# Kernel optimization log

Measured on AMD Instinct MI355X. Metric: run time of the kernel, lower is better.

## Reference

```python
import jax, jax.numpy as jnp
import numpy as np


def setup_inputs() -> dict:
    key = jax.random.key(0)
    k1, k2, k3, k4 = jax.random.split(key, 4)
    B, S, E = 8, 4096, 1024
    H, D = 256, 4  # num_heads, n_wires_per_head; H*D == E
    scale = 1.0 / np.sqrt(E)
    return {
        "x": jax.random.normal(k1, (B, S, E), dtype=jnp.float32),
        "W_proj": jax.random.normal(k2, (E, E), dtype=jnp.float32) * scale,
        "W_combine": jax.random.normal(k3, (E, E), dtype=jnp.float32) * scale,
        "phi": jax.random.normal(k4, (H, D), dtype=jnp.float32),
    }


def reference(x, W_proj, W_combine, phi):
    # Linear projection (no bias): torch Linear computes x @ W.T
    proj = jnp.einsum("bse,fe->bsf", x, W_proj)  # [B,S,E]
    B, S, E = proj.shape
    H, D = phi.shape
    # Quantum head per token: RX-encode each feature, trainable RX, PauliZ measure.
    # RX(a)RX(b) = RX(a+b); <0|RX(t)^dag Z RX(t)|0> = cos(t)  =>  cos(x + phi)
    qout = jnp.cos(proj.reshape(B, S, H, D) + phi)  # broadcast phi[h,d]
    qout = qout.reshape(B, S, E)
    return jnp.einsum("bse,fe->bsf", qout, W_combine)
```

## Files before the change

### kernel.cpp

```cpp
#include <hip/hip_runtime.h>
#include <cstdint>
#include <cstddef>


typedef __attribute__((ext_vector_type(8))) short short8;
typedef __attribute__((ext_vector_type(4))) float f32x4;

__device__ __forceinline__ unsigned short f2bf(float f) {
  unsigned u = __float_as_uint(f);
  u += 0x7FFFu + ((u >> 16) & 1u);
  return (unsigned short)(u >> 16);
}

__device__ __forceinline__ void async_load16(const void* g, const void* l) {
  __builtin_amdgcn_global_load_lds(
      (const __attribute__((address_space(1))) void*)g,
      (__attribute__((address_space(3))) void*)l,
      16, 0, 0);
}

__global__ __launch_bounds__(256) void cast_all(
    const float* __restrict__ x, const float* __restrict__ Wp,
    const float* __restrict__ Wc, unsigned short* __restrict__ xb,
    unsigned short* __restrict__ wpb, unsigned short* __restrict__ wcb) {
  long i = ((long)blockIdx.x * 256 + threadIdx.x) * 4;
  const float* s;
  unsigned short* d;
  long j;
  if (i < 33554432)      { s = x;  d = xb;  j = i; }
  else if (i < 34603008) { s = Wp; d = wpb; j = i - 33554432; }
  else                   { s = Wc; d = wcb; j = i - 34603008; }
  const float4 v = *(const float4*)(s + j);
  ushort4 o;
  o.x = f2bf(v.x); o.y = f2bf(v.y); o.z = f2bf(v.z); o.w = f2bf(v.w);
  *(ushort4*)(d + j) = o;
}

constexpr int TM = 128, TN = 128, BK = 32;
constexpr int Kdim = 1024, Ndim = 1024;

template <int EPI>
__global__ __launch_bounds__(256, 2) void gemm_bt(
    const unsigned short* __restrict__ A,
    const unsigned short* __restrict__ B,
    const float* __restrict__ phi,
    void* __restrict__ Cout) {
  __shared__ unsigned short As[TM * BK];
  __shared__ unsigned short Bs[TN * BK];

  const int tid  = threadIdx.x;
  const int lane = tid & 63;
  const int wv   = tid >> 6;
  const int m_blk = blockIdx.x & 255;
  const int n_blk = blockIdx.x >> 8;
  const long row0 = (long)m_blk * TM;
  const int  col0 = n_blk * TN;

  const int s_row  = lane >> 2;
  const int s_colb = (lane & 3) * 16;

  const int lane15 = lane & 15;
  const int quad   = lane >> 4;
  const int wm = (wv >> 1) * 64;
  const int wn = (wv & 1) * 64;

  f32x4 acc[4][4];
#pragma unroll
  for (int mi = 0; mi < 4; ++mi)
#pragma unroll
    for (int ni = 0; ni < 4; ++ni) {
      f32x4 z = {0.f, 0.f, 0.f, 0.f};
      acc[mi][ni] = z;
    }

  for (int k0 = 0; k0 < Kdim; k0 += BK) {
#pragma unroll
    for (int j = 0; j < 2; ++j) {
      const int chunk = wv * 2 + j;
      const int row = chunk * 16 + s_row;
      const char* ga = (const char*)(A + (row0 + row) * Kdim + k0) + s_colb;
      async_load16(ga, (const char*)As + chunk * 1024);
      const char* gb = (const char*)(B + (long)(col0 + row) * Kdim + k0) + s_colb;
      async_load16(gb, (const char*)Bs + chunk * 1024);
    }
    __syncthreads();

    short8 af[4], bfr[4];
#pragma unroll
    for (int mi = 0; mi < 4; ++mi)
      af[mi] = *(const short8*)(As + (wm + mi * 16 + lane15) * BK + quad * 8);
#pragma unroll
    for (int ni = 0; ni < 4; ++ni)
      bfr[ni] = *(const short8*)(Bs + (wn + ni * 16 + lane15) * BK + quad * 8);
#pragma unroll
    for (int mi = 0; mi < 4; ++mi)
#pragma unroll
      for (int ni = 0; ni < 4; ++ni)
        acc[mi][ni] = __builtin_amdgcn_mfma_f32_16x16x32_bf16(
            af[mi], bfr[ni], acc[mi][ni], 0, 0, 0);
    __syncthreads();
  }

  if (EPI == 1) {
    unsigned short* Q = (unsigned short*)Cout;
    float ph[4];
#pragma unroll
    for (int ni = 0; ni < 4; ++ni)
      ph[ni] = phi[col0 + wn + ni * 16 + lane15];
#pragma unroll
    for (int mi = 0; mi < 4; ++mi) {
      const long rbase = row0 + wm + mi * 16 + quad * 4;
#pragma unroll
      for (int ni = 0; ni < 4; ++ni) {
        const int c = col0 + wn + ni * 16 + lane15;
#pragma unroll
        for (int r = 0; r < 4; ++r) {
          float v = __cosf(acc[mi][ni][r] + ph[ni]);
          Q[(rbase + r) * Ndim + c] = f2bf(v);
        }
      }
    }
  } else {
    float* C = (float*)Cout;
#pragma unroll
    for (int mi = 0; mi < 4; ++mi) {
      const long rbase = row0 + wm + mi * 16 + quad * 4;
#pragma unroll
      for (int ni = 0; ni < 4; ++ni) {
        const int c = col0 + wn + ni * 16 + lane15;
#pragma unroll
        for (int r = 0; r < 4; ++r)
          C[(rbase + r) * Ndim + c] = acc[mi][ni][r];
      }
    }
  }
}

extern "C" void kernel_launch(void* const* d_in, const int* in_sizes, int n_in,
                              void* d_out, int out_size, void* d_ws, size_t ws_size,
                              hipStream_t stream) {
  const float* x   = (const float*)d_in[0];
  const float* Wp  = (const float*)d_in[1];
  const float* Wc  = (const float*)d_in[2];
  const float* phi = (const float*)d_in[3];
  float* out = (float*)d_out;

  char* ws = (char*)d_ws;
  unsigned short* Abf  = (unsigned short*)(ws);
  unsigned short* Qbf  = (unsigned short*)(ws + (size_t)67108864);
  unsigned short* Wpbf = (unsigned short*)(ws + (size_t)134217728);
  unsigned short* Wcbf = (unsigned short*)(ws + (size_t)136314880);

  cast_all<<<34816, 256, 0, stream>>>(x, Wp, Wc, Abf, Wpbf, Wcbf);
  gemm_bt<1><<<2048, 256, 0, stream>>>(Abf, Wpbf, phi, (void*)Qbf);
  gemm_bt<0><<<2048, 256, 0, stream>>>(Qbf, Wcbf, nullptr, (void*)out);

  (void)in_sizes; (void)n_in; (void)out_size; (void)ws_size;
}
```

Measured before the change: 386.1 us.

## Rewrite GEMM as 256x256 double-buffered tile with swizzled LDS and interleaved MFMA

Replaces the 128x128 single-buffered GEMM with a 256x256 tile, BK=64, 512 threads and a two-stage LDS double buffer. The next K tile is prefetched while MFMAs run, using explicit vmcnt waits, and priority is raised around the MFMA blocks. It adds an XOR swizzle on LDS rows to avoid bank conflicts and remaps blocks to improve L2 locality. The cost is many barriers per iteration, more LDS and registers per block, and fewer blocks in flight (512 instead of 2048).

After: 396.6 us. 2.7% more time.

```diff
diff --git a/kernel.cpp b/kernel.cpp
--- a/kernel.cpp
+++ b/kernel.cpp
@@ -36,86 +36,172 @@
   *(ushort4*)(d + j) = o;
 }
 
-constexpr int TM = 128, TN = 128, BK = 32;
+constexpr int BM = 256, BN = 256, BK = 64;
 constexpr int Kdim = 1024, Ndim = 1024;
+constexpr int KT = Kdim / BK;
 
 template <int EPI>
-__global__ __launch_bounds__(256, 2) void gemm_bt(
+__global__ __launch_bounds__(512, 2) void gemm256(
     const unsigned short* __restrict__ A,
     const unsigned short* __restrict__ B,
     const float* __restrict__ phi,
     void* __restrict__ Cout) {
-  __shared__ unsigned short As[TM * BK];
-  __shared__ unsigned short Bs[TN * BK];
-
-  const int tid  = threadIdx.x;
-  const int lane = tid & 63;
-  const int wv   = tid >> 6;
-  const int m_blk = blockIdx.x & 255;
-  const int n_blk = blockIdx.x >> 8;
-  const long row0 = (long)m_blk * TM;
-  const int  col0 = n_blk * TN;
-
-  const int s_row  = lane >> 2;
-  const int s_colb = (lane & 3) * 16;
-
+  __shared__ unsigned short As[2][2][256][32];
+  __shared__ unsigned short Bs[2][2][256][32];
+
+  const int tid    = threadIdx.x;
+  const int lane   = tid & 63;
+  const int wv     = tid >> 6;
+  const int wr     = wv >> 2;
+  const int wc     = wv & 3;
   const int lane15 = lane & 15;
   const int quad   = lane >> 4;
-  const int wm = (wv >> 1) * 64;
-  const int wn = (wv & 1) * 64;
-
-  f32x4 acc[4][4];
-#pragma unroll
-  for (int mi = 0; mi < 4; ++mi)
-#pragma unroll
-    for (int ni = 0; ni < 4; ++ni) {
+  const int swz8   = (quad ^ ((lane15 >> 1) & 3)) * 8;
+
+  const int wg   = ((blockIdx.x & 7) << 6) | (blockIdx.x >> 3);
+  const long row0 = (long)(wg >> 2) * BM;
+  const int  col0 = (wg & 3) * BN;
+
+  const int rsub  = lane >> 2;
+  const int csrc8 = ((lane & 3) ^ ((lane >> 3) & 3)) * 8;
+  const int rA    = wv * 32 + rsub;
+
+#define STAGE(KTIDX, NB)                                                      \
+  {                                                                           \
+    const unsigned short* ga0 = A + (row0 + rA) * Kdim + (KTIDX) * BK + csrc8;\
+    const unsigned short* ga1 = ga0 + (long)16 * Kdim;                        \
+    const unsigned short* gb0 =                                               \
+        B + (long)(col0 + rA) * Kdim + (KTIDX) * BK + csrc8;                  \
+    const unsigned short* gb1 = gb0 + (long)16 * Kdim;                        \
+    _Pragma("unroll")                                                         \
+    for (int kh = 0; kh < 2; ++kh) {                                          \
+      async_load16(ga0 + kh * 32, &As[NB][kh][wv * 32][0]);                   \
+      async_load16(ga1 + kh * 32, &As[NB][kh][wv * 32 + 16][0]);              \
+      async_load16(gb0 + kh * 32, &Bs[NB][kh][wv * 32][0]);                   \
+      async_load16(gb1 + kh * 32, &Bs[NB][kh][wv * 32 + 16][0]);              \
+    }                                                                         \
+  }
+
+  f32x4 acc[8][4];
+#pragma unroll
+  for (int i = 0; i < 8; ++i)
+#pragma unroll
+    for (int n = 0; n < 4; ++n) {
       f32x4 z = {0.f, 0.f, 0.f, 0.f};
-      acc[mi][ni] = z;
-    }
-
-  for (int k0 = 0; k0 < Kdim; k0 += BK) {
-#pragma unroll
-    for (int j = 0; j < 2; ++j) {
-      const int chunk = wv * 2 + j;
-      const int row = chunk * 16 + s_row;
-      const char* ga = (const char*)(A + (row0 + row) * Kdim + k0) + s_colb;
-      async_load16(ga, (const char*)As + chunk * 1024);
-      const char* gb = (const char*)(B + (long)(col0 + row) * Kdim + k0) + s_colb;
-      async_load16(gb, (const char*)Bs + chunk * 1024);
-    }
-    __syncthreads();
-
+      acc[i][n] = z;
+    }
+
+  STAGE(0, 0);
+  asm volatile("s_waitcnt vmcnt(4)" ::: "memory");
+  __builtin_amdgcn_s_barrier();
+
+#pragma unroll 2
+  for (int kt = 0; kt < KT; ++kt) {
+    const int cur = kt & 1;
     short8 af[4], bfr[4];
-#pragma unroll
-    for (int mi = 0; mi < 4; ++mi)
-      af[mi] = *(const short8*)(As + (wm + mi * 16 + lane15) * BK + quad * 8);
-#pragma unroll
-    for (int ni = 0; ni < 4; ++ni)
-      bfr[ni] = *(const short8*)(Bs + (wn + ni * 16 + lane15) * BK + quad * 8);
-#pragma unroll
-    for (int mi = 0; mi < 4; ++mi)
-#pragma unroll
-      for (int ni = 0; ni < 4; ++ni)
-        acc[mi][ni] = __builtin_amdgcn_mfma_f32_16x16x32_bf16(
-            af[mi], bfr[ni], acc[mi][ni], 0, 0, 0);
-    __syncthreads();
+
+#pragma unroll
+    for (int i = 0; i < 4; ++i)
+      af[i] = *(const short8*)(&As[cur][0][wr * 128 + i * 16 + lane15][swz8]);
+#pragma unroll
+    for (int i = 0; i < 4; ++i)
+      bfr[i] = *(const short8*)(&Bs[cur][0][wc * 64 + i * 16 + lane15][swz8]);
+    if (kt + 1 < KT) STAGE(kt + 1, cur ^ 1);
+    __builtin_amdgcn_s_barrier();
+    asm volatile("s_waitcnt lgkmcnt(0)" ::: "memory");
+    __builtin_amdgcn_sched_barrier(0);
+    __builtin_amdgcn_s_setprio(1);
+#pragma unroll
+    for (int i = 0; i < 4; ++i)
+#pragma unroll
+      for (int n = 0; n < 4; ++n)
+        acc[i][n] = __builtin_amdgcn_mfma_f32_16x16x32_bf16(
+            af[i], bfr[n], acc[i][n], 0, 0, 0);
+    __builtin_amdgcn_s_setprio(0);
+    __builtin_amdgcn_sched_barrier(0);
+    __builtin_amdgcn_s_barrier();
+
+#pragma unroll
+    for (int i = 0; i < 4; ++i)
+      af[i] =
+          *(const short8*)(&As[cur][0][wr * 128 + (4 + i) * 16 + lane15][swz8]);
+    __builtin_amdgcn_s_barrier();
+    asm volatile("s_waitcnt lgkmcnt(0)" ::: "memory");
+    __builtin_amdgcn_sched_barrier(0);
+    __builtin_amdgcn_s_setprio(1);
+#pragma unroll
+    for (int i = 0; i < 4; ++i)
+#pragma unroll
+      for (int n = 0; n < 4; ++n)
+        acc[4 + i][n] = __builtin_amdgcn_mfma_f32_16x16x32_bf16(
+            af[i], bfr[n], acc[4 + i][n], 0, 0, 0);
+    __builtin_amdgcn_s_setprio(0);
+    __builtin_amdgcn_sched_barrier(0);
+    if (kt == KT - 1) {
+      asm volatile("s_waitcnt vmcnt(0)" ::: "memory");
+    } else {
+      asm volatile("s_waitcnt vmcnt(8)" ::: "memory");
+    }
+    __builtin_amdgcn_s_barrier();
+
+#pragma unroll
+    for (int i = 0; i < 4; ++i)
+      af[i] = *(const short8*)(&As[cur][1][wr * 128 + i * 16 + lane15][swz8]);
+#pragma unroll
+    for (int i = 0; i < 4; ++i)
+      bfr[i] = *(const short8*)(&Bs[cur][1][wc * 64 + i * 16 + lane15][swz8]);
+    __builtin_amdgcn_s_barrier();
+    asm volatile("s_waitcnt lgkmcnt(0)" ::: "memory");
+    __builtin_amdgcn_sched_barrier(0);
+    __builtin_amdgcn_s_setprio(1);
+#pragma unroll
+    for (int i = 0; i < 4; ++i)
+#pragma unroll
+      for (int n = 0; n < 4; ++n)
+        acc[i][n] = __builtin_amdgcn_mfma_f32_16x16x32_bf16(
+            af[i], bfr[n], acc[i][n], 0, 0, 0);
+    __builtin_amdgcn_s_setprio(0);
+    __builtin_amdgcn_sched_barrier(0);
+    __builtin_amdgcn_s_barrier();
+
+#pragma unroll
+    for (int i = 0; i < 4; ++i)
+      af[i] =
+          *(const short8*)(&As[cur][1][wr * 128 + (4 + i) * 16 + lane15][swz8]);
+    __builtin_amdgcn_s_barrier();
+    asm volatile("s_waitcnt lgkmcnt(0)" ::: "memory");
+    __builtin_amdgcn_sched_barrier(0);
+    __builtin_amdgcn_s_setprio(1);
+#pragma unroll
+    for (int i = 0; i < 4; ++i)
+#pragma unroll
+      for (int n = 0; n < 4; ++n)
+        acc[4 + i][n] = __builtin_amdgcn_mfma_f32_16x16x32_bf16(
+            af[i], bfr[n], acc[4 + i][n], 0, 0, 0);
+    __builtin_amdgcn_s_setprio(0);
+    __builtin_amdgcn_sched_barrier(0);
+    if (kt < KT - 1) {
+      asm volatile("s_waitcnt vmcnt(4)" ::: "memory");
+    }
+    __builtin_amdgcn_s_barrier();
   }
+#undef STAGE
 
   if (EPI == 1) {
     unsigned short* Q = (unsigned short*)Cout;
     float ph[4];
 #pragma unroll
-    for (int ni = 0; ni < 4; ++ni)
-      ph[ni] = phi[col0 + wn + ni * 16 + lane15];
-#pragma unroll
-    for (int mi = 0; mi < 4; ++mi) {
-      const long rbase = row0 + wm + mi * 16 + quad * 4;
-#pragma unroll
-      for (int ni = 0; ni < 4; ++ni) {
-        const int c = col0 + wn + ni * 16 + lane15;
+    for (int n = 0; n < 4; ++n)
+      ph[n] = phi[col0 + wc * 64 + n * 16 + lane15];
+#pragma unroll
+    for (int mi = 0; mi < 8; ++mi) {
+      const long rbase = row0 + wr * 128 + mi * 16 + quad * 4;
+#pragma unroll
+      for (int n = 0; n < 4; ++n) {
+        const int c = col0 + wc * 64 + n * 16 + lane15;
 #pragma unroll
         for (int r = 0; r < 4; ++r) {
-          float v = __cosf(acc[mi][ni][r] + ph[ni]);
+          float v = __cosf(acc[mi][n][r] + ph[n]);
           Q[(rbase + r) * Ndim + c] = f2bf(v);
         }
       }
@@ -123,14 +209,14 @@
   } else {
     float* C = (float*)Cout;
 #pragma unroll
-    for (int mi = 0; mi < 4; ++mi) {
-      const long rbase = row0 + wm + mi * 16 + quad * 4;
-#pragma unroll
-      for (int ni = 0; ni < 4; ++ni) {
-        const int c = col0 + wn + ni * 16 + lane15;
+    for (int mi = 0; mi < 8; ++mi) {
+      const long rbase = row0 + wr * 128 + mi * 16 + quad * 4;
+#pragma unroll
+      for (int n = 0; n < 4; ++n) {
+        const int c = col0 + wc * 64 + n * 16 + lane15;
 #pragma unroll
         for (int r = 0; r < 4; ++r)
-          C[(rbase + r) * Ndim + c] = acc[mi][ni][r];
+          C[(rbase + r) * Ndim + c] = acc[mi][n][r];
       }
     }
   }
@@ -152,8 +238,8 @@
   unsigned short* Wcbf = (unsigned short*)(ws + (size_t)136314880);
 
   cast_all<<<34816, 256, 0, stream>>>(x, Wp, Wc, Abf, Wpbf, Wcbf);
-  gemm_bt<1><<<2048, 256, 0, stream>>>(Abf, Wpbf, phi, (void*)Qbf);
-  gemm_bt<0><<<2048, 256, 0, stream>>>(Qbf, Wcbf, nullptr, (void*)out);
+  gemm256<1><<<512, 512, 0, stream>>>(Abf, Wpbf, phi, (void*)Qbf);
+  gemm256<0><<<512, 512, 0, stream>>>(Qbf, Wcbf, nullptr, (void*)out);
 
   (void)in_sizes; (void)n_in; (void)out_size; (void)ws_size;
 }
```
